# Performance work log

Measured on AMD Instinct MI355X. Metric: run time of the kernel, lower is better.

## Reference

```python
import jax, jax.numpy as jnp
import numpy as np

B, IN, H = 16384, 512, 512


def setup_inputs() -> dict:
    key = jax.random.key(0)
    ks = jax.random.split(key, 7)
    s_in = 1.0 / np.sqrt(IN)
    s_h = 1.0 / np.sqrt(H)
    return {
        "x": jax.random.normal(ks[0], (B, IN), jnp.float32),
        "h": jax.random.normal(ks[1], (B, H), jnp.float32),
        "c": jax.random.normal(ks[2], (B, H), jnp.float32),
        # packed gate weights, order [i, f, g, o] along last dim (4*H)
        "Wx": jax.random.normal(ks[3], (IN, 4 * H), jnp.float32) * s_in,
        "Wh": jax.random.normal(ks[4], (H, 4 * H), jnp.float32) * s_h,
        "bx": jax.random.normal(ks[5], (4 * H,), jnp.float32) * s_in,
        "bh": jax.random.normal(ks[6], (4 * H,), jnp.float32) * s_h,
    }


def reference(x, h, c, Wx, Wh, bx, bh):
    # one fused GEMM per input stream instead of 8 small linears; same math
    gates = x @ Wx + bx + h @ Wh + bh          # [B, 4H]
    gi, gf, gg, go = jnp.split(gates, 4, axis=-1)
    i = jax.nn.sigmoid(gi)
    f = jax.nn.sigmoid(gf)
    g = jnp.tanh(gg)
    o = jax.nn.sigmoid(go)
    c_new = f * c + i * g
    h_new = o * jnp.tanh(c_new)
    return (h_new, c_new)
```

## Files before the change

### kernel.cpp

```cpp
#include <hip/hip_runtime.h>
#include <hip/hip_bf16.h>

#define B_DIM   16384
#define IN_DIM  512
#define H_DIM   512
#define K_DIM   1024
#define N4H     2048
#define BH      (B_DIM * H_DIM)

typedef __attribute__((ext_vector_type(8))) short  short8;
typedef __attribute__((ext_vector_type(4))) short  short4v;
typedef __attribute__((ext_vector_type(4))) float  f32x4;

__device__ inline void async_load16(const void* g, void* l) {
    __builtin_amdgcn_global_load_lds(
        (const __attribute__((address_space(1))) void*)g,
        (__attribute__((address_space(3)))       void*)l, 16, 0, 0);
}

__device__ inline short bf16bits(float f) {
    __hip_bfloat16 b = __float2bfloat16(f);
    return *reinterpret_cast<short*>(&b);
}

__device__ inline float sigmoidf_(float v) {
    return 1.0f / (1.0f + __expf(-v));
}
__device__ inline float tanhf_(float v) {
    v = fminf(fmaxf(v, -30.f), 30.f);
    float e = __expf(2.f * v);
    return (e - 1.f) / (e + 1.f);
}

__global__ __launch_bounds__(256) void prep_all(
    const float* __restrict__ Wx, const float* __restrict__ Wh,
    const float* __restrict__ bx, const float* __restrict__ bh,
    const float* __restrict__ x,  const float* __restrict__ h,
    __hip_bfloat16* __restrict__ Wt, __hip_bfloat16* __restrict__ Axh,
    float* __restrict__ bias_p) {
    const int bid = blockIdx.x;
    const int t   = threadIdx.x;

    if (bid < 2048) {
        __shared__ __hip_bfloat16 tile[32][33];
        const int bk = bid & 31;
        const int bn = bid >> 5;
        const int kb = bk * 32, nb = bn * 32;
#pragma unroll
        for (int r = 0; r < 4; ++r) {
            int k_loc = r * 8 + (t >> 5);
            int n_loc = t & 31;
            int kg = kb + k_loc;
            float v = (kg < IN_DIM) ? Wx[(size_t)kg * N4H + nb + n_loc]
                                    : Wh[(size_t)(kg - IN_DIM) * N4H + nb + n_loc];
            tile[k_loc][n_loc] = __float2bfloat16(v);
        }
        __syncthreads();
        {
            int n_loc = t >> 3;
            int k_loc = (t & 7) * 4;
            int ng = nb + n_loc;
            int g  = ng >> 9;
            int c  = ng & 511;
            int row_out = (c >> 5) * 128 + g * 32 + (c & 31);
            short4v v4;
            v4.x = *reinterpret_cast<short*>(&tile[k_loc + 0][n_loc]);
            v4.y = *reinterpret_cast<short*>(&tile[k_loc + 1][n_loc]);
            v4.z = *reinterpret_cast<short*>(&tile[k_loc + 2][n_loc]);
            v4.w = *reinterpret_cast<short*>(&tile[k_loc + 3][n_loc]);
            *(short4v*)&Wt[(size_t)row_out * K_DIM + kb + k_loc] = v4;
        }
        if (bid < 8) {
            int ng = bid * 256 + t;
            int g  = ng >> 9;
            int c  = ng & 511;
            int ro = (c >> 5) * 128 + g * 32 + (c & 31);
            bias_p[ro] = bx[ng] + bh[ng];
        }
    } else {
        const int ab = bid - 2048;
        const int kq = t;
        const float* src = (kq < 128) ? (x + kq * 4)
                                      : (h + (size_t)(kq - 128) * 4);
#pragma unroll
        for (int j = 0; j < 8; ++j) {
            int m = ab * 8 + j;
            float4 v = *(const float4*)(src + (size_t)m * 512);
            short4v sv;
            sv.x = bf16bits(v.x);
            sv.y = bf16bits(v.y);
            sv.z = bf16bits(v.z);
            sv.w = bf16bits(v.w);
            *(short4v*)&Axh[(size_t)m * K_DIM + kq * 4] = sv;
        }
    }
}

__global__ __launch_bounds__(256, 3) void lstm_gemm(
    const float* __restrict__ c_in,
    const __hip_bfloat16* __restrict__ Axh,
    const __hip_bfloat16* __restrict__ Wt,
    const float* __restrict__ bias_p,
    float* __restrict__ out) {
    __shared__ __align__(16) unsigned char smem[32768];

    const int tid   = threadIdx.x;
    const int w     = tid >> 6;
    const int lane  = tid & 63;
    const int col16 = lane & 15;
    const int quad  = lane >> 4;
    const int wm    = w >> 1;
    const int wn    = w & 1;

    const int jb    = blockIdx.x;
    const int xcd   = jb & 7;
    const int local = jb >> 3;
    const int bm    = xcd * 16 + (local >> 4);
    const int bn    = local & 15;

    f32x4 acc[4][4];
#pragma unroll
    for (int mi = 0; mi < 4; ++mi)
#pragma unroll
        for (int ni = 0; ni < 4; ++ni)
            acc[mi][ni] = (f32x4){0.f, 0.f, 0.f, 0.f};

    const __hip_bfloat16* Ab = Axh + (size_t)bm * 128 * K_DIM;
    const __hip_bfloat16* Bb = Wt  + (size_t)bn * 128 * K_DIM;

    const int s0 = w * 128 + lane;
    const int s1 = s0 + 64;
    const int r0 = s0 >> 2, r1 = s1 >> 2;
    const int q0 = ((s0 & 3) - ((r0 >> 1) & 3)) & 3;
    const int q1 = ((s1 & 3) - ((r1 >> 1) & 3)) & 3;
    const size_t ga0 = (size_t)r0 * K_DIM + q0 * 8;
    const size_t ga1 = (size_t)r1 * K_DIM + q1 * 8;

    int aoff[4], boff[4];
#pragma unroll
    for (int mi = 0; mi < 4; ++mi) {
        int r = wm * 64 + mi * 16 + col16;
        aoff[mi] = (r * 4 + ((quad + ((r >> 1) & 3)) & 3)) * 16;
    }
#pragma unroll
    for (int ni = 0; ni < 4; ++ni) {
        int r = wn * 64 + ni * 16 + col16;
        boff[ni] = (r * 4 + ((quad + ((r >> 1) & 3)) & 3)) * 16;
    }

    char* sbase = (char*)smem;

    async_load16(Ab + ga0, sbase + w * 2048);
    async_load16(Ab + ga1, sbase + w * 2048 + 1024);
    async_load16(Bb + ga0, sbase + 8192 + w * 2048);
    async_load16(Bb + ga1, sbase + 8192 + w * 2048 + 1024);

    for (int kt = 0; kt < 32; ++kt) {
        __syncthreads();
        const int p = kt & 1;
        if (kt < 31) {
            const int kb = (kt + 1) * 32;
            char* nb_ = sbase + (1 - p) * 16384;
            async_load16(Ab + ga0 + kb, nb_ + w * 2048);
            async_load16(Ab + ga1 + kb, nb_ + w * 2048 + 1024);
            async_load16(Bb + ga0 + kb, nb_ + 8192 + w * 2048);
            async_load16(Bb + ga1 + kb, nb_ + 8192 + w * 2048 + 1024);
        }
        const char* lap = sbase + p * 16384;
        const char* lbp = lap + 8192;

        short8 afr[4], bfr[4];
#pragma unroll
        for (int mi = 0; mi < 4; ++mi)
            afr[mi] = *(const short8*)(lap + aoff[mi]);
#pragma unroll
        for (int ni = 0; ni < 4; ++ni)
            bfr[ni] = *(const short8*)(lbp + boff[ni]);
#pragma unroll
        for (int mi = 0; mi < 4; ++mi)
#pragma unroll
            for (int ni = 0; ni < 4; ++ni)
                acc[mi][ni] = __builtin_amdgcn_mfma_f32_16x16x32_bf16(
                    afr[mi], bfr[ni], acc[mi][ni], 0, 0, 0);
    }

    __syncthreads();
    float* fx = (float*)smem;

    if (wn == 1) {
        float bg[2][2];
#pragma unroll
        for (int g2 = 0; g2 < 2; ++g2)
#pragma unroll
            for (int hh = 0; hh < 2; ++hh)
                bg[g2][hh] = bias_p[bn * 128 + (2 + g2) * 32 + hh * 16 + col16];
#pragma unroll
        for (int mi = 0; mi < 4; ++mi)
#pragma unroll
            for (int ni = 0; ni < 4; ++ni) {
                int g2 = ni >> 1, hh = ni & 1;
                int hc = hh * 16 + col16;
#pragma unroll
                for (int reg = 0; reg < 4; ++reg) {
                    int row = wm * 64 + mi * 16 + quad * 4 + reg;
                    int sw = (hc + ((row >> 2) & 3) * 8) & 31;
                    fx[g2 * 4096 + row * 32 + sw] = acc[mi][ni][reg] + bg[g2][hh];
                }
            }
    }
    __syncthreads();
    if (wn == 0) {
        float bi[2][2];
#pragma unroll
        for (int g = 0; g < 2; ++g)
#pragma unroll
            for (int hh = 0; hh < 2; ++hh)
                bi[g][hh] = bias_p[bn * 128 + g * 32 + hh * 16 + col16];
#pragma unroll
        for (int mi = 0; mi < 4; ++mi)
#pragma unroll
            for (int reg = 0; reg < 4; ++reg) {
                int row = wm * 64 + mi * 16 + quad * 4 + reg;
                size_t m_g = (size_t)(bm * 128 + row);
                int swb = ((row >> 2) & 3) * 8;
#pragma unroll
                for (int hh = 0; hh < 2; ++hh) {
                    int hc = hh * 16 + col16;
                    int sw = (hc + swb) & 31;
                    float gi = acc[mi][0 + hh][reg] + bi[0][hh];
                    float gf = acc[mi][2 + hh][reg] + bi[1][hh];
                    float gg = fx[row * 32 + sw];
                    float go = fx[4096 + row * 32 + sw];
                    float iv = sigmoidf_(gi);
                    float fv = sigmoidf_(gf);
                    float gv = tanhf_(gg);
                    float ov = sigmoidf_(go);
                    int col = bn * 32 + hc;
                    float co = c_in[m_g * H_DIM + col];
                    float cn = fv * co + iv * gv;
                    float hn = ov * tanhf_(cn);
                    out[m_g * H_DIM + col]      = hn;
                    out[BH + m_g * H_DIM + col] = cn;
                }
            }
    }
}

__global__ __launch_bounds__(256) void prep_weights_fb(
    const float* __restrict__ Wx, const float* __restrict__ Wh,
    const float* __restrict__ bx, const float* __restrict__ bh,
    __hip_bfloat16* __restrict__ Wt, float* __restrict__ bias_p) {
    __shared__ __hip_bfloat16 tile[32][33];
    const int bid = blockIdx.x;
    const int bk  = bid & 31;
    const int bn  = bid >> 5;
    const int t   = threadIdx.x;
    const int kb  = bk * 32, nb = bn * 32;
#pragma unroll
    for (int r = 0; r < 4; ++r) {
        int k_loc = r * 8 + (t >> 5);
        int n_loc = t & 31;
        int kg = kb + k_loc;
        float v = (kg < IN_DIM) ? Wx[(size_t)kg * N4H + nb + n_loc]
                                : Wh[(size_t)(kg - IN_DIM) * N4H + nb + n_loc];
        tile[k_loc][n_loc] = __float2bfloat16(v);
    }
    __syncthreads();
    {
        int n_loc = t >> 3;
        int k_loc = (t & 7) * 4;
        int ng = nb + n_loc;
        int g  = ng >> 9;
        int c  = ng & 511;
        int row_out = (c >> 5) * 128 + g * 32 + (c & 31);
        short4v v4;
        v4.x = *reinterpret_cast<short*>(&tile[k_loc + 0][n_loc]);
        v4.y = *reinterpret_cast<short*>(&tile[k_loc + 1][n_loc]);
        v4.z = *reinterpret_cast<short*>(&tile[k_loc + 2][n_loc]);
        v4.w = *reinterpret_cast<short*>(&tile[k_loc + 3][n_loc]);
        *(short4v*)&Wt[(size_t)row_out * K_DIM + kb + k_loc] = v4;
    }
    if (bid < 8) {
        int ng = bid * 256 + t;
        int g  = ng >> 9;
        int c  = ng & 511;
        int ro = (c >> 5) * 128 + g * 32 + (c & 31);
        bias_p[ro] = bx[ng] + bh[ng];
    }
}

__global__ __launch_bounds__(256, 3) void lstm_gemm_fb(
    const float* __restrict__ x, const float* __restrict__ h,
    const float* __restrict__ c_in,
    const __hip_bfloat16* __restrict__ Wt, const float* __restrict__ bias_p,
    float* __restrict__ out) {
    __shared__ __hip_bfloat16 lds_a[128 * 32];
    __shared__ __hip_bfloat16 lds_b[128 * 32];
    const int tid   = threadIdx.x;
    const int bn    = blockIdx.x & 15;
    const int bm    = blockIdx.x >> 4;
    const int w     = tid >> 6;
    const int lane  = tid & 63;
    const int col16 = lane & 15;
    const int quad  = lane >> 4;
    f32x4 acc[2][8];
#pragma unroll
    for (int mi = 0; mi < 2; ++mi)
#pragma unroll
        for (int ni = 0; ni < 8; ++ni)
            acc[mi][ni] = (f32x4){0.f, 0.f, 0.f, 0.f};
    const __hip_bfloat16* wt_base = Wt + (size_t)(bn * 128) * K_DIM;
    const int chunk0 = w * 2;
    const int e0     = chunk0 * 512 + lane * 8;
    const int bn_loc0 = e0 >> 5, bk_off0 = e0 & 31;
    const int e1     = (chunk0 + 1) * 512 + lane * 8;
    const int bn_loc1 = e1 >> 5, bk_off1 = e1 & 31;
    for (int kt = 0; kt < 32; ++kt) {
        const int kb = kt * 32;
        const float* aptr;
        int koff;
        if (kb < IN_DIM) { aptr = x; koff = kb; }
        else             { aptr = h; koff = kb - IN_DIM; }
        async_load16(wt_base + (size_t)bn_loc0 * K_DIM + kb + bk_off0,
                     (void*)(lds_b + chunk0 * 512));
        async_load16(wt_base + (size_t)bn_loc1 * K_DIM + kb + bk_off1,
                     (void*)(lds_b + (chunk0 + 1) * 512));
        float4 av[4];
#pragma unroll
        for (int j = 0; j < 4; ++j) {
            int cch = j * 256 + tid;
            int row = cch >> 3;
            int kq  = (cch & 7) * 4;
            av[j] = *(const float4*)(aptr + (size_t)(bm * 128 + row) * IN_DIM
                                     + koff + kq);
        }
#pragma unroll
        for (int j = 0; j < 4; ++j) {
            int cch = j * 256 + tid;
            int row = cch >> 3;
            int kq  = (cch & 7) * 4;
            short4v sv;
            sv.x = bf16bits(av[j].x);
            sv.y = bf16bits(av[j].y);
            sv.z = bf16bits(av[j].z);
            sv.w = bf16bits(av[j].w);
            *(short4v*)&lds_a[row * 32 + kq] = sv;
        }
        __syncthreads();
        short8 afr[2], bfr[8];
#pragma unroll
        for (int mi = 0; mi < 2; ++mi)
            afr[mi] = *(const short8*)&lds_a[(w * 32 + mi * 16 + col16) * 32 + quad * 8];
#pragma unroll
        for (int ni = 0; ni < 8; ++ni)
            bfr[ni] = *(const short8*)&lds_b[(ni * 16 + col16) * 32 + quad * 8];
#pragma unroll
        for (int mi = 0; mi < 2; ++mi)
#pragma unroll
            for (int ni = 0; ni < 8; ++ni)
                acc[mi][ni] = __builtin_amdgcn_mfma_f32_16x16x32_bf16(
                    afr[mi], bfr[ni], acc[mi][ni], 0, 0, 0);
        __syncthreads();
    }
    float bias_v[4][2];
#pragma unroll
    for (int g = 0; g < 4; ++g)
#pragma unroll
        for (int h2 = 0; h2 < 2; ++h2)
            bias_v[g][h2] = bias_p[bn * 128 + g * 32 + h2 * 16 + col16];
#pragma unroll
    for (int mi = 0; mi < 2; ++mi) {
#pragma unroll
        for (int reg = 0; reg < 4; ++reg) {
            const int m_g = bm * 128 + w * 32 + mi * 16 + quad * 4 + reg;
#pragma unroll
            for (int h2 = 0; h2 < 2; ++h2) {
                const int hc_g = bn * 32 + h2 * 16 + col16;
                float gi = acc[mi][0 + h2][reg] + bias_v[0][h2];
                float gf = acc[mi][2 + h2][reg] + bias_v[1][h2];
                float gg = acc[mi][4 + h2][reg] + bias_v[2][h2];
                float go = acc[mi][6 + h2][reg] + bias_v[3][h2];
                float iv = sigmoidf_(gi);
                float fv = sigmoidf_(gf);
                float gv = tanhf_(gg);
                float ov = sigmoidf_(go);
                float co = c_in[(size_t)m_g * H_DIM + hc_g];
                float cn = fv * co + iv * gv;
                float hn = ov * tanhf_(cn);
                out[(size_t)m_g * H_DIM + hc_g]      = hn;
                out[BH + (size_t)m_g * H_DIM + hc_g] = cn;
            }
        }
    }
}

extern "C" void kernel_launch(void* const* d_in, const int* in_sizes, int n_in,
                              void* d_out, int out_size, void* d_ws, size_t ws_size,
                              hipStream_t stream) {
    const float* x  = (const float*)d_in[0];
    const float* h  = (const float*)d_in[1];
    const float* c  = (const float*)d_in[2];
    const float* Wx = (const float*)d_in[3];
    const float* Wh = (const float*)d_in[4];
    const float* bx = (const float*)d_in[5];
    const float* bh = (const float*)d_in[6];

    const size_t wtBytes  = (size_t)N4H * K_DIM * 2;
    const size_t axhBytes = (size_t)B_DIM * K_DIM * 2;
    const size_t need     = wtBytes + axhBytes + (size_t)N4H * 4;

    if (ws_size >= need) {
        __hip_bfloat16* Wt  = (__hip_bfloat16*)d_ws;
        __hip_bfloat16* Axh = (__hip_bfloat16*)((char*)d_ws + wtBytes);
        float* bias_p = (float*)((char*)d_ws + wtBytes + axhBytes);
        prep_all<<<4096, 256, 0, stream>>>(Wx, Wh, bx, bh, x, h, Wt, Axh, bias_p);
        lstm_gemm<<<2048, 256, 0, stream>>>(c, Axh, Wt, bias_p, (float*)d_out);
    } else {
        __hip_bfloat16* Wt = (__hip_bfloat16*)d_ws;
        float* bias_p = (float*)((char*)d_ws + wtBytes);
        prep_weights_fb<<<2048, 256, 0, stream>>>(Wx, Wh, bx, bh, Wt, bias_p);
        lstm_gemm_fb<<<2048, 256, 0, stream>>>(x, h, c, Wt, bias_p, (float*)d_out);
    }
}
```

Measured before the change: 253.7 us.

## Shrink GEMM tile to 64x128 for higher occupancy and remap block-to-XCD order

The main fused GEMM tile drops from 128x128 to 64x128 rows, which halves the accumulators and cuts shared memory to 24KB so occupancy can rise from 3 to 5 blocks per CU, with twice as many blocks launched. Block indexing changes so each XCD owns two weight column tiles and walks through all row tiles, aiming for weight reuse in each XCD's L2. The async load distribution is rewritten to three 16-byte loads per thread covering the A and B tiles. In exchange, each loaded B tile is reused across fewer MFMAs, so global and LDS traffic per flop goes up.

```diff
diff --git a/kernel.cpp b/kernel.cpp
--- a/kernel.cpp
+++ b/kernel.cpp
@@ -96,13 +96,13 @@
     }
 }
 
-__global__ __launch_bounds__(256, 3) void lstm_gemm(
+__global__ __launch_bounds__(256, 5) void lstm_gemm(
     const float* __restrict__ c_in,
     const __hip_bfloat16* __restrict__ Axh,
     const __hip_bfloat16* __restrict__ Wt,
     const float* __restrict__ bias_p,
     float* __restrict__ out) {
-    __shared__ __align__(16) unsigned char smem[32768];
+    __shared__ __align__(16) unsigned char smem[24576];
 
     const int tid   = threadIdx.x;
     const int w     = tid >> 6;
@@ -115,69 +115,74 @@
     const int jb    = blockIdx.x;
     const int xcd   = jb & 7;
     const int local = jb >> 3;
-    const int bm    = xcd * 16 + (local >> 4);
-    const int bn    = local & 15;
-
-    f32x4 acc[4][4];
-#pragma unroll
-    for (int mi = 0; mi < 4; ++mi)
+    const int bn    = xcd * 2 + (local & 1);
+    const int bm    = local >> 1;
+
+    f32x4 acc[2][4];
+#pragma unroll
+    for (int mi = 0; mi < 2; ++mi)
 #pragma unroll
         for (int ni = 0; ni < 4; ++ni)
             acc[mi][ni] = (f32x4){0.f, 0.f, 0.f, 0.f};
 
-    const __hip_bfloat16* Ab = Axh + (size_t)bm * 128 * K_DIM;
+    const __hip_bfloat16* Ab = Axh + (size_t)bm * 64 * K_DIM;
     const __hip_bfloat16* Bb = Wt  + (size_t)bn * 128 * K_DIM;
 
-    const int s0 = w * 128 + lane;
-    const int s1 = s0 + 64;
-    const int r0 = s0 >> 2, r1 = s1 >> 2;
-    const int q0 = ((s0 & 3) - ((r0 >> 1) & 3)) & 3;
-    const int q1 = ((s1 & 3) - ((r1 >> 1) & 3)) & 3;
-    const size_t ga0 = (size_t)r0 * K_DIM + q0 * 8;
-    const size_t ga1 = (size_t)r1 * K_DIM + q1 * 8;
-
-    int aoff[4], boff[4];
-#pragma unroll
-    for (int mi = 0; mi < 4; ++mi) {
-        int r = wm * 64 + mi * 16 + col16;
+    const __hip_bfloat16* gsrc[3];
+    size_t goff[3];
+    int    ldst[3];
+#pragma unroll
+    for (int j = 0; j < 3; ++j) {
+        int idx = w * 3 + j;
+        int s   = idx * 64 + lane;
+        int isB = (idx >= 4);
+        int sl  = isB ? (s - 256) : s;
+        int r   = sl >> 2;
+        int q   = ((sl & 3) - ((r >> 1) & 3)) & 3;
+        gsrc[j] = isB ? Bb : Ab;
+        goff[j] = (size_t)r * K_DIM + q * 8;
+        ldst[j] = (isB ? 4096 : 0) + (isB ? (idx - 4) : idx) * 1024;
+    }
+
+    int aoff[2], boff[4];
+#pragma unroll
+    for (int mi = 0; mi < 2; ++mi) {
+        int r = wm * 32 + mi * 16 + col16;
         aoff[mi] = (r * 4 + ((quad + ((r >> 1) & 3)) & 3)) * 16;
     }
 #pragma unroll
     for (int ni = 0; ni < 4; ++ni) {
         int r = wn * 64 + ni * 16 + col16;
-        boff[ni] = (r * 4 + ((quad + ((r >> 1) & 3)) & 3)) * 16;
+        boff[ni] = 4096 + (r * 4 + ((quad + ((r >> 1) & 3)) & 3)) * 16;
     }
 
     char* sbase = (char*)smem;
 
-    async_load16(Ab + ga0, sbase + w * 2048);
-    async_load16(Ab + ga1, sbase + w * 2048 + 1024);
-    async_load16(Bb + ga0, sbase + 8192 + w * 2048);
-    async_load16(Bb + ga1, sbase + 8192 + w * 2048 + 1024);
+#pragma unroll
+    for (int j = 0; j < 3; ++j)
+        async_load16(gsrc[j] + goff[j], sbase + ldst[j]);
 
     for (int kt = 0; kt < 32; ++kt) {
         __syncthreads();
         const int p = kt & 1;
         if (kt < 31) {
             const int kb = (kt + 1) * 32;
-            char* nb_ = sbase + (1 - p) * 16384;
-            async_load16(Ab + ga0 + kb, nb_ + w * 2048);
-            async_load16(Ab + ga1 + kb, nb_ + w * 2048 + 1024);
-            async_load16(Bb + ga0 + kb, nb_ + 8192 + w * 2048);
-            async_load16(Bb + ga1 + kb, nb_ + 8192 + w * 2048 + 1024);
-        }
-        const char* lap = sbase + p * 16384;
-        const char* lbp = lap + 8192;
-
-        short8 afr[4], bfr[4];
-#pragma unroll
-        for (int mi = 0; mi < 4; ++mi)
-            afr[mi] = *(const short8*)(lap + aoff[mi]);
+            char* nb_ = sbase + (1 - p) * 12288;
+#pragma unroll
+            for (int j = 0; j < 3; ++j)
+                async_load16(gsrc[j] + goff[j] + kb, nb_ + ldst[j]);
+        }
+        const char* lp = sbase + p * 12288;
+
+        short8 afr[2], bfr[4];
+#pragma unroll
+        for (int mi = 0; mi < 2; ++mi)
+            afr[mi] = *(const short8*)(lp + aoff[mi]);
 #pragma unroll
         for (int ni = 0; ni < 4; ++ni)
-            bfr[ni] = *(const short8*)(lbp + boff[ni]);
-#pragma unroll
-        for (int mi = 0; mi < 4; ++mi)
+            bfr[ni] = *(const short8*)(lp + boff[ni]);
+#pragma unroll
+        for (int mi = 0; mi < 2; ++mi)
 #pragma unroll
             for (int ni = 0; ni < 4; ++ni)
                 acc[mi][ni] = __builtin_amdgcn_mfma_f32_16x16x32_bf16(
@@ -195,16 +200,16 @@
             for (int hh = 0; hh < 2; ++hh)
                 bg[g2][hh] = bias_p[bn * 128 + (2 + g2) * 32 + hh * 16 + col16];
 #pragma unroll
-        for (int mi = 0; mi < 4; ++mi)
+        for (int mi = 0; mi < 2; ++mi)
 #pragma unroll
             for (int ni = 0; ni < 4; ++ni) {
                 int g2 = ni >> 1, hh = ni & 1;
                 int hc = hh * 16 + col16;
 #pragma unroll
                 for (int reg = 0; reg < 4; ++reg) {
-                    int row = wm * 64 + mi * 16 + quad * 4 + reg;
+                    int row = wm * 32 + mi * 16 + quad * 4 + reg;
                     int sw = (hc + ((row >> 2) & 3) * 8) & 31;
-                    fx[g2 * 4096 + row * 32 + sw] = acc[mi][ni][reg] + bg[g2][hh];
+                    fx[g2 * 2048 + row * 32 + sw] = acc[mi][ni][reg] + bg[g2][hh];
                 }
             }
     }
@@ -217,11 +222,11 @@
             for (int hh = 0; hh < 2; ++hh)
                 bi[g][hh] = bias_p[bn * 128 + g * 32 + hh * 16 + col16];
 #pragma unroll
-        for (int mi = 0; mi < 4; ++mi)
+        for (int mi = 0; mi < 2; ++mi)
 #pragma unroll
             for (int reg = 0; reg < 4; ++reg) {
-                int row = wm * 64 + mi * 16 + quad * 4 + reg;
-                size_t m_g = (size_t)(bm * 128 + row);
+                int row = wm * 32 + mi * 16 + quad * 4 + reg;
+                size_t m_g = (size_t)(bm * 64 + row);
                 int swb = ((row >> 2) & 3) * 8;
 #pragma unroll
                 for (int hh = 0; hh < 2; ++hh) {
@@ -230,7 +235,7 @@
                     float gi = acc[mi][0 + hh][reg] + bi[0][hh];
                     float gf = acc[mi][2 + hh][reg] + bi[1][hh];
                     float gg = fx[row * 32 + sw];
-                    float go = fx[4096 + row * 32 + sw];
+                    float go = fx[2048 + row * 32 + sw];
                     float iv = sigmoidf_(gi);
                     float fv = sigmoidf_(gf);
                     float gv = tanhf_(gg);
@@ -414,7 +419,7 @@
         __hip_bfloat16* Axh = (__hip_bfloat16*)((char*)d_ws + wtBytes);
         float* bias_p = (float*)((char*)d_ws + wtBytes + axhBytes);
         prep_all<<<4096, 256, 0, stream>>>(Wx, Wh, bx, bh, x, h, Wt, Axh, bias_p);
-        lstm_gemm<<<2048, 256, 0, stream>>>(c, Axh, Wt, bias_p, (float*)d_out);
+        lstm_gemm<<<4096, 256, 0, stream>>>(c, Axh, Wt, bias_p, (float*)d_out);
     } else {
         __hip_bfloat16* Wt = (__hip_bfloat16*)d_ws;
         float* bias_p = (float*)((char*)d_ws + wtBytes);
```

Result: slower. 269.7 us (+6.3%).
